# Kernel optimization log

Measured on AMD Instinct MI355X. Metric: run time of the kernel, lower is better.

Reference implementation:

```python
import jax, jax.numpy as jnp
import numpy as np

N, E, G, H = 4096, 8192, 64, 128  # nodes, edges, graphs, hidden dim
NODE_DIM, EDGE_DIM = 11, 5


def _linear_params(key, fan_in, fan_out):
    kw, kb = jax.random.split(key)
    s = 1.0 / np.sqrt(fan_in)
    w = jax.random.uniform(kw, (fan_in, fan_out), minval=-s, maxval=s, dtype=jnp.float32)
    b = jax.random.uniform(kb, (fan_out,), minval=-s, maxval=s, dtype=jnp.float32)
    return w, b


def setup_inputs() -> dict:
    key = jax.random.key(0)
    ks = jax.random.split(key, 10)
    x = jax.random.normal(ks[0], (N, NODE_DIM), dtype=jnp.float32)
    edge_attr = jax.random.normal(ks[1], (E, EDGE_DIM), dtype=jnp.float32)
    edge_index = jax.random.randint(ks[2], (2, E), 0, N, dtype=jnp.int64)
    batch = jnp.sort(jax.random.randint(ks[3], (N,), 0, G, dtype=jnp.int64))
    # preprocess MLP: node_dim -> 128 -> 128
    p1_w, p1_b = _linear_params(ks[4], NODE_DIM, H)
    p2_w, p2_b = _linear_params(ks[5], H, H)
    # edge net: edge_dim -> 128 -> 256 -> 128 -> 128*128 (ReLU between, none after last)
    e1_w, e1_b = _linear_params(ks[6], EDGE_DIM, 128)
    e2_w, e2_b = _linear_params(ks[7], 128, 256)
    e3_w, e3_b = _linear_params(ks[8], 256, 128)
    e4_w, e4_b = _linear_params(ks[9], 128, H * H)
    return {"x": x, "edge_attr": edge_attr, "edge_index": edge_index, "batch": batch,
            "p1_w": p1_w, "p1_b": p1_b, "p2_w": p2_w, "p2_b": p2_b,
            "e1_w": e1_w, "e1_b": e1_b, "e2_w": e2_w, "e2_b": e2_b,
            "e3_w": e3_w, "e3_b": e3_b, "e4_w": e4_w, "e4_b": e4_b}


def reference(x, edge_attr, edge_index, batch,
              p1_w, p1_b, p2_w, p2_b,
              e1_w, e1_b, e2_w, e2_b, e3_w, e3_b, e4_w, e4_b):
    # node preprocess MLP (maps 11-dim features to 128 so NNConv dims are consistent)
    h = jax.nn.relu(x @ p1_w + p1_b) @ p2_w + p2_b  # [N, H]
    # edge network -> per-edge weight matrix [E, H, H]
    e = jax.nn.relu(edge_attr @ e1_w + e1_b)
    e = jax.nn.relu(e @ e2_w + e2_b)
    e = jax.nn.relu(e @ e3_w + e3_b)
    W = (e @ e4_w + e4_b).reshape(E, H, H)
    # NNConv (root_weight=False, bias=False, aggr='mean'):
    src, dst = edge_index[0], edge_index[1]
    msg = jnp.einsum('ei,eio->eo', h[src], W)  # gather + per-edge matmul, [E, H]
    agg = jax.ops.segment_sum(msg, dst, num_segments=N)
    cnt = jax.ops.segment_sum(jnp.ones((E,), msg.dtype), dst, num_segments=N)
    h_out = agg / jnp.maximum(cnt, 1.0)[:, None]  # scatter-mean, [N, H]
    # global add pool over graphs
    pooled = jax.ops.segment_sum(h_out, batch, num_segments=G)  # [G, H]
    return pooled
```

## Files before the change

kernel.cpp:

```cpp
#include <hip/hip_runtime.h>
#include <stdint.h>
#include <stddef.h>

typedef unsigned short ushort_t;
typedef __attribute__((ext_vector_type(8))) short short8;
typedef __attribute__((ext_vector_type(4))) short short4v;
typedef __attribute__((ext_vector_type(4))) float f32x4;

#define GL2LDS(gsrc, ldst) \
  __builtin_amdgcn_global_load_lds((const __attribute__((address_space(1))) void*)(gsrc), \
                                   (__attribute__((address_space(3))) void*)(ldst), 16, 0, 0)

__device__ __forceinline__ float bf2f(ushort_t u) {
  union { unsigned int i; float f; } v; v.i = ((unsigned int)u) << 16; return v.f;
}
__device__ __forceinline__ ushort_t f2bf(float f) {
  unsigned int u = __builtin_bit_cast(unsigned int, f);
  unsigned int r = (u + 0x7fffu + ((u >> 16) & 1u)) >> 16;
  return (ushort_t)r;
}

__global__ void k_front(const float* __restrict__ e4w, const float* __restrict__ e4b,
                        ushort_t* __restrict__ e4wT,
                        const float* __restrict__ e2w, ushort_t* __restrict__ w2h,
                        ushort_t* __restrict__ w2l,
                        const float* __restrict__ e3w, ushort_t* __restrict__ w3h,
                        ushort_t* __restrict__ w3l,
                        const float* __restrict__ x, const float* __restrict__ p1w,
                        const float* __restrict__ p1b, const float* __restrict__ p2w,
                        const float* __restrict__ p2b, ushort_t* __restrict__ h_node) {
  __shared__ char smem[128 * 65 * 4];
  int bid = blockIdx.x, tid = threadIdx.x;

  if (bid < 258) {
    float (*t)[65] = (float(*)[65])smem;
    int c0 = bid * 64;
    for (int it = 0; it < 32; ++it) {
      int idx = it * 256 + tid;
      int cc = idx >> 7, oo = idx & 127;
      int c = c0 + cc;
      float v = (c < 16384) ? e4w[(size_t)c * 128 + oo] : e4b[(size_t)(c - 16384) * 128 + oo];
      t[oo][cc] = v;
    }
    __syncthreads();
    for (int it = 0; it < 32; ++it) {
      int idx = it * 256 + tid;
      int oo = idx >> 6, cc = idx & 63;
      e4wT[(size_t)oo * 16512 + c0 + cc] = f2bf(t[oo][cc]);
    }
  } else if (bid < 274) {
    int id = (bid - 258) * 256 + tid;
    int cf = id >> 8, ks = (id >> 6) & 3, ln = id & 63;
    int n = cf * 16 + (ln & 15);
    int k0 = (ks * 4 + (ln >> 4)) * 8;
    short8 ph, pl;
#pragma unroll
    for (int q = 0; q < 8; ++q) {
      float v = e2w[(size_t)(k0 + q) * 256 + n];
      ushort_t hb = f2bf(v);
      ph[q] = (short)hb;
      pl[q] = (short)f2bf(v - bf2f(hb));
    }
    *(short8*)(w2h + (size_t)id * 8) = ph;
    *(short8*)(w2l + (size_t)id * 8) = pl;
  } else if (bid < 290) {
    int id = (bid - 274) * 256 + tid;
    int cf = id >> 9, ks = (id >> 6) & 7, ln = id & 63;
    int n = cf * 16 + (ln & 15);
    int k0 = (ks * 4 + (ln >> 4)) * 8;
    short8 ph, pl;
#pragma unroll
    for (int q = 0; q < 8; ++q) {
      float v = e3w[(size_t)(k0 + q) * 128 + n];
      ushort_t hb = f2bf(v);
      ph[q] = (short)hb;
      pl[q] = (short)f2bf(v - bf2f(hb));
    }
    *(short8*)(w3h + (size_t)id * 8) = ph;
    *(short8*)(w3l + (size_t)id * 8) = pl;
  } else {
    float (*xs)[12] = (float(*)[12])smem;
    float (*t1)[128] = (float(*)[128])(smem + 8 * 12 * 4);
    int n0 = (bid - 290) * 8;
    if (tid < 88) { int n = tid / 11, j = tid % 11; xs[n][j] = x[(size_t)(n0 + n) * 11 + j]; }
    __syncthreads();
    for (int it = 0; it < 4; ++it) {
      int p = it * 256 + tid;
      int n = p >> 7, o = p & 127;
      float a = p1b[o];
#pragma unroll
      for (int j = 0; j < 11; ++j) a += xs[n][j] * p1w[j * 128 + o];
      t1[n][o] = fmaxf(a, 0.f);
    }
    __syncthreads();
    {
      int o = tid & 127, nb = tid >> 7;
      float a0 = p2b[o], a1_ = a0, a2_ = a0, a3_ = a0;
      for (int k4 = 0; k4 < 32; ++k4) {
        float w0 = p2w[(k4 * 4 + 0) * 128 + o];
        float w1 = p2w[(k4 * 4 + 1) * 128 + o];
        float w2 = p2w[(k4 * 4 + 2) * 128 + o];
        float w3 = p2w[(k4 * 4 + 3) * 128 + o];
        float4 v0 = *(const float4*)&t1[nb + 0][k4 * 4];
        float4 v1 = *(const float4*)&t1[nb + 2][k4 * 4];
        float4 v2 = *(const float4*)&t1[nb + 4][k4 * 4];
        float4 v3 = *(const float4*)&t1[nb + 6][k4 * 4];
        a0 += v0.x * w0 + v0.y * w1 + v0.z * w2 + v0.w * w3;
        a1_ += v1.x * w0 + v1.y * w1 + v1.z * w2 + v1.w * w3;
        a2_ += v2.x * w0 + v2.y * w1 + v2.z * w2 + v2.w * w3;
        a3_ += v3.x * w0 + v3.y * w1 + v3.z * w2 + v3.w * w3;
      }
      h_node[(size_t)(n0 + nb + 0) * 128 + o] = f2bf(a0);
      h_node[(size_t)(n0 + nb + 2) * 128 + o] = f2bf(a1_);
      h_node[(size_t)(n0 + nb + 4) * 128 + o] = f2bf(a2_);
      h_node[(size_t)(n0 + nb + 6) * 128 + o] = f2bf(a3_);
    }
  }
}

__global__ void k_mlp(const float* __restrict__ ea,
                      const float* __restrict__ e1w, const float* __restrict__ e1b,
                      const ushort_t* __restrict__ w2h, const ushort_t* __restrict__ w2l,
                      const float* __restrict__ e2b,
                      const ushort_t* __restrict__ w3h, const ushort_t* __restrict__ w3l,
                      const float* __restrict__ e3b,
                      float* __restrict__ e3Tf) {
  __shared__ float eas[32][6];
  __shared__ ushort_t a1h[32 * 136], a1l[32 * 136];
  __shared__ ushort_t a2h[32 * 264], a2l[32 * 264];
  __shared__ float a3t[128 * 40];

  int tid = threadIdx.x;
  int w = tid >> 6, ln = tid & 63, g = ln >> 4, l15 = ln & 15;
  int e0 = blockIdx.x * 32;

  if (tid < 160) { int n = tid / 5, j = tid % 5; eas[n][j] = ea[(size_t)(e0 + n) * 5 + j]; }
  __syncthreads();

  {
    int n = tid >> 4, ob = (tid & 15) * 8;
    float acc1[8];
    float4 ba = *(const float4*)(e1b + ob);
    float4 bb = *(const float4*)(e1b + ob + 4);
    acc1[0] = ba.x; acc1[1] = ba.y; acc1[2] = ba.z; acc1[3] = ba.w;
    acc1[4] = bb.x; acc1[5] = bb.y; acc1[6] = bb.z; acc1[7] = bb.w;
#pragma unroll
    for (int j = 0; j < 5; ++j) {
      float aj = eas[n][j];
      float4 wa = *(const float4*)(e1w + j * 128 + ob);
      float4 wb = *(const float4*)(e1w + j * 128 + ob + 4);
      acc1[0] = fmaf(aj, wa.x, acc1[0]); acc1[1] = fmaf(aj, wa.y, acc1[1]);
      acc1[2] = fmaf(aj, wa.z, acc1[2]); acc1[3] = fmaf(aj, wa.w, acc1[3]);
      acc1[4] = fmaf(aj, wb.x, acc1[4]); acc1[5] = fmaf(aj, wb.y, acc1[5]);
      acc1[6] = fmaf(aj, wb.z, acc1[6]); acc1[7] = fmaf(aj, wb.w, acc1[7]);
    }
    short8 ph, pl;
#pragma unroll
    for (int q = 0; q < 8; ++q) {
      float v = fmaxf(acc1[q], 0.f);
      ushort_t hb = f2bf(v);
      ph[q] = (short)hb;
      pl[q] = (short)f2bf(v - bf2f(hb));
    }
    int addr = n * 136 + ob;
    *(short8*)(a1h + addr) = ph;
    *(short8*)(a1l + addr) = pl;
  }
  __syncthreads();

  {
    f32x4 acc2[2][2];
#pragma unroll
    for (int rf = 0; rf < 2; ++rf)
#pragma unroll
      for (int cf = 0; cf < 2; ++cf) acc2[rf][cf] = (f32x4){0.f, 0.f, 0.f, 0.f};
    short8 ah[2][4], al[2][4];
#pragma unroll
    for (int rf = 0; rf < 2; ++rf)
#pragma unroll
      for (int ks = 0; ks < 4; ++ks) {
        int row = rf * 16 + l15;
        int addr = row * 136 + (ks * 4 + g) * 8;
        ah[rf][ks] = *(const short8*)(a1h + addr);
        al[rf][ks] = *(const short8*)(a1l + addr);
      }
#pragma unroll
    for (int ks = 0; ks < 4; ++ks) {
#pragma unroll
      for (int cfi = 0; cfi < 2; ++cfi) {
        int cf = w * 2 + cfi;
        size_t poff = (size_t)(((cf * 4 + ks) << 6) + ln) * 8;
        short8 bh = *(const short8*)(w2h + poff);
        short8 bl = *(const short8*)(w2l + poff);
#pragma unroll
        for (int rf = 0; rf < 2; ++rf) {
          acc2[rf][cfi] = __builtin_amdgcn_mfma_f32_16x16x32_bf16(ah[rf][ks], bh, acc2[rf][cfi], 0, 0, 0);
          acc2[rf][cfi] = __builtin_amdgcn_mfma_f32_16x16x32_bf16(al[rf][ks], bh, acc2[rf][cfi], 0, 0, 0);
          acc2[rf][cfi] = __builtin_amdgcn_mfma_f32_16x16x32_bf16(ah[rf][ks], bl, acc2[rf][cfi], 0, 0, 0);
        }
      }
    }
#pragma unroll
    for (int rf = 0; rf < 2; ++rf)
#pragma unroll
      for (int cfi = 0; cfi < 2; ++cfi) {
        int col = (w * 2 + cfi) * 16 + l15;
        float b = e2b[col];
#pragma unroll
        for (int r2 = 0; r2 < 4; ++r2) {
          int row = rf * 16 + g * 4 + r2;
          float v = fmaxf(acc2[rf][cfi][r2] + b, 0.f);
          ushort_t hb = f2bf(v);
          int addr = row * 264 + col;
          a2h[addr] = hb;
          a2l[addr] = f2bf(v - bf2f(hb));
        }
      }
  }
  __syncthreads();

  {
    f32x4 acc3[2];
    acc3[0] = (f32x4){0.f, 0.f, 0.f, 0.f};
    acc3[1] = (f32x4){0.f, 0.f, 0.f, 0.f};
#pragma unroll
    for (int ks = 0; ks < 8; ++ks) {
      short8 a2hf[2], a2lf[2];
#pragma unroll
      for (int rf = 0; rf < 2; ++rf) {
        int row = rf * 16 + l15;
        int addr = row * 264 + (ks * 4 + g) * 8;
        a2hf[rf] = *(const short8*)(a2h + addr);
        a2lf[rf] = *(const short8*)(a2l + addr);
      }
      size_t poff = (size_t)(((w * 8 + ks) << 6) + ln) * 8;
      short8 bh = *(const short8*)(w3h + poff);
      short8 bl = *(const short8*)(w3l + poff);
#pragma unroll
      for (int rf = 0; rf < 2; ++rf) {
        acc3[rf] = __builtin_amdgcn_mfma_f32_16x16x32_bf16(a2hf[rf], bh, acc3[rf], 0, 0, 0);
        acc3[rf] = __builtin_amdgcn_mfma_f32_16x16x32_bf16(a2lf[rf], bh, acc3[rf], 0, 0, 0);
        acc3[rf] = __builtin_amdgcn_mfma_f32_16x16x32_bf16(a2hf[rf], bl, acc3[rf], 0, 0, 0);
      }
    }
    int col = w * 16 + l15;
    float b = e3b[col];
#pragma unroll
    for (int rf = 0; rf < 2; ++rf)
#pragma unroll
      for (int r2 = 0; r2 < 4; ++r2) {
        int row = rf * 16 + g * 4 + r2;
        float v = fmaxf(acc3[rf][r2] + b, 0.f);
        a3t[col * 40 + row] = v;
      }
  }
  __syncthreads();

  {
    int o = tid >> 2, eq = (tid & 3) * 8;
    float4 q0 = *(const float4*)(a3t + o * 40 + eq);
    float4 q1 = *(const float4*)(a3t + o * 40 + eq + 4);
    *(float4*)(e3Tf + (size_t)o * 8192 + e0 + eq) = q0;
    *(float4*)(e3Tf + (size_t)o * 8192 + e0 + eq + 4) = q1;
  }
}

__launch_bounds__(512, 1)
__global__ void k_gemm(const ushort_t* __restrict__ h_node, const int* __restrict__ eidx,
                       const float* __restrict__ e3Tf,
                       const ushort_t* __restrict__ e4wT, ushort_t* __restrict__ partial) {
  __shared__ ushort_t bufA[16384];
  __shared__ float e3s[32 * 128];

  int tid = threadIdx.x;
  int w = tid >> 6, ln = tid & 63;
  int g = ln >> 4, l15 = ln & 15;
  int bid = blockIdx.x;
  int mt = bid >> 2, s = bid & 3;
  int e0 = mt * 128;
  int t0 = s * 32;
  int nt = (s == 3) ? 33 : 32;

  {
#pragma unroll
    for (int it = 0; it < 4; ++it) {
      int chunk = it * 512 + tid;
      int r = chunk >> 4;
      int Gt = (chunk & 15) ^ (r & 15);
      int se = eidx[e0 + r];
      GL2LDS(h_node + (size_t)se * 128 + Gt * 8, (char*)&bufA[0] + (it * 512 + w * 64) * 16);
    }
#pragma unroll
    for (int it = 0; it < 2; ++it) {
      int chunk = it * 512 + tid;
      int tl = chunk >> 5, cc = chunk & 31;
      GL2LDS(e3Tf + (size_t)(t0 + tl) * 8192 + e0 + cc * 4,
             (char*)&e3s[0] + (it * 512 + w * 64) * 16);
    }
  }
  asm volatile("s_waitcnt vmcnt(0)" ::: "memory");
  __builtin_amdgcn_s_barrier();
  asm volatile("" ::: "memory");

  short8 afr[8][4];
#pragma unroll
  for (int rf = 0; rf < 8; ++rf)
#pragma unroll
    for (int ks = 0; ks < 4; ++ks) {
      int row = rf * 16 + l15;
      int gr = (ks * 4 + g) ^ (row & 15);
      afr[rf][ks] = *(const short8*)((const char*)&bufA[0] + row * 256 + gr * 16);
    }

  f32x4 acc[8];
#pragma unroll
  for (int rf = 0; rf < 8; ++rf) acc[rf] = (f32x4){0.f, 0.f, 0.f, 0.f};

  const f32x4 zero4 = {0.f, 0.f, 0.f, 0.f};
  int nrow = w * 16 + l15;

  const ushort_t* brow = e4wT + (size_t)nrow * 16512 + (size_t)t0 * 128;
  short8 bcur[4], bnxt[4];
#pragma unroll
  for (int ks = 0; ks < 4; ++ks) bcur[ks] = *(const short8*)(brow + (ks * 4 + g) * 8);
  brow += 128;

  for (int tl = 0; tl < nt; ++tl) {
    int tg = t0 + tl;

    if (tl + 1 < nt) {
#pragma unroll
      for (int ks = 0; ks < 4; ++ks) bnxt[ks] = *(const short8*)(brow + (ks * 4 + g) * 8);
      brow += 128;
    }

    f32x4 part[8];
#pragma unroll
    for (int rf = 0; rf < 8; ++rf)
      part[rf] = __builtin_amdgcn_mfma_f32_16x16x32_bf16(afr[rf][0], bcur[0], zero4, 0, 0, 0);
#pragma unroll
    for (int ks = 1; ks < 4; ++ks)
#pragma unroll
      for (int rf = 0; rf < 8; ++rf)
        part[rf] = __builtin_amdgcn_mfma_f32_16x16x32_bf16(afr[rf][ks], bcur[ks], part[rf], 0, 0, 0);

    if (tg < 128) {
#pragma unroll
      for (int rf = 0; rf < 8; ++rf) {
        float4 ev = *(const float4*)&e3s[tl * 128 + rf * 16 + g * 4];
        acc[rf][0] = fmaf(ev.x, part[rf][0], acc[rf][0]);
        acc[rf][1] = fmaf(ev.y, part[rf][1], acc[rf][1]);
        acc[rf][2] = fmaf(ev.z, part[rf][2], acc[rf][2]);
        acc[rf][3] = fmaf(ev.w, part[rf][3], acc[rf][3]);
      }
    } else {
#pragma unroll
      for (int rf = 0; rf < 8; ++rf)
#pragma unroll
        for (int r2 = 0; r2 < 4; ++r2) acc[rf][r2] += part[rf][r2];
    }

    if (tl + 1 < nt) {
#pragma unroll
      for (int ks = 0; ks < 4; ++ks) bcur[ks] = bnxt[ks];
    }
  }

#pragma unroll
  for (int rf = 0; rf < 8; ++rf)
#pragma unroll
    for (int r2 = 0; r2 < 4; ++r2) {
      int row = rf * 16 + g * 4 + r2;
      partial[((size_t)s * 8192 + e0 + row) * 128 + nrow] = f2bf(acc[rf][r2]);
    }
}

__global__ void k_reduce(const ushort_t* __restrict__ partial, const int* __restrict__ eidx,
                         float* __restrict__ agg, float* __restrict__ cnt) {
  int id = blockIdx.x * 256 + threadIdx.x;
  int e = id >> 4, oc = (id & 15) * 8;
  float v[8];
#pragma unroll
  for (int q = 0; q < 8; ++q) v[q] = 0.f;
#pragma unroll
  for (int s2 = 0; s2 < 4; ++s2) {
    short8 p = *(const short8*)(partial + ((size_t)s2 * 8192 + e) * 128 + oc);
#pragma unroll
    for (int q = 0; q < 8; ++q) v[q] += bf2f((ushort_t)p[q]);
  }
  int d = eidx[8192 + e];
  float* dst = agg + (size_t)d * 128 + oc;
#pragma unroll
  for (int q = 0; q < 8; ++q) atomicAdd(dst + q, v[q]);
  if ((id & 15) == 0) atomicAdd(&cnt[d], 1.0f);
}

__device__ __forceinline__ int lbound(const int* a, int n, int v) {
  int lo = 0, hi = n;
  while (lo < hi) { int m = (lo + hi) >> 1; if (a[m] < v) lo = m + 1; else hi = m; }
  return lo;
}

__global__ void k_pool(const float* __restrict__ agg, const float* __restrict__ cnt,
                       const int* __restrict__ batch, float* __restrict__ out) {
  int gph = blockIdx.x, o = threadIdx.x;
  int lo = lbound(batch, 4096, gph);
  int hi = lbound(batch, 4096, gph + 1);
  float a = 0.f;
  for (int n = lo; n < hi; ++n) a += agg[(size_t)n * 128 + o] / fmaxf(cnt[n], 1.0f);
  out[(size_t)gph * 128 + o] = a;
}

extern "C" void kernel_launch(void* const* d_in, const int* in_sizes, int n_in,
                              void* d_out, int out_size, void* d_ws, size_t ws_size,
                              hipStream_t stream) {
  (void)in_sizes; (void)n_in; (void)out_size; (void)ws_size;
  const float* x   = (const float*)d_in[0];
  const float* ea  = (const float*)d_in[1];
  const int*   ei  = (const int*)d_in[2];
  const int*   bat = (const int*)d_in[3];
  const float* p1w = (const float*)d_in[4];  const float* p1b = (const float*)d_in[5];
  const float* p2w = (const float*)d_in[6];  const float* p2b = (const float*)d_in[7];
  const float* e1w = (const float*)d_in[8];  const float* e1b = (const float*)d_in[9];
  const float* e2w = (const float*)d_in[10]; const float* e2b = (const float*)d_in[11];
  const float* e3w = (const float*)d_in[12]; const float* e3b = (const float*)d_in[13];
  const float* e4w = (const float*)d_in[14]; const float* e4b = (const float*)d_in[15];

  char* ws = (char*)d_ws;
  ushort_t* e4wT   = (ushort_t*)(ws + 0);
  ushort_t* h_node = (ushort_t*)(ws + 4227072);
  float*    e3Tf   = (float*)(ws + 5275648);
  ushort_t* part   = (ushort_t*)(ws + 9469952);
  float*    agg    = (float*)(ws + 17858560);
  float*    cnt    = (float*)(ws + 19955712);
  ushort_t* w2h    = (ushort_t*)(ws + 19972096);
  ushort_t* w2l    = (ushort_t*)(ws + 20037632);
  ushort_t* w3h    = (ushort_t*)(ws + 20103168);
  ushort_t* w3l    = (ushort_t*)(ws + 20168704);

  hipMemsetAsync(ws + 17858560, 0, 2097152 + 16384, stream);

  k_front <<<802,  256, 0, stream>>>(e4w, e4b, e4wT, e2w, w2h, w2l, e3w, w3h, w3l,
                                     x, p1w, p1b, p2w, p2b, h_node);
  k_mlp   <<<256,  512, 0, stream>>>(ea, e1w, e1b, w2h, w2l, e2b,
                                     w3h, w3l, e3b, e3Tf);
  k_gemm  <<<256,  512, 0, stream>>>(h_node, ei, e3Tf, e4wT, part);
  k_reduce<<<512,  256, 0, stream>>>(part, ei, agg, cnt);
  k_pool  <<<64,   128, 0, stream>>>(agg, cnt, bat, (float*)d_out);
}
```

Measured before the change: 204.5 us.

## Retile edge GEMM to 64-edge blocks with 16 waves split 2x8

Halves the edge tile per block from 128 to 64 rows and raises the block to 1024 threads (16 waves arranged 2 along edges by 8 along output columns), doubling the grid to 512 blocks. Each wave now holds 2 A fragments instead of 8, cutting register pressure and raising occupancy across the CUs. The cost is that every B fragment of the large e4wT weight is now streamed by twice as many blocks, so there is less reuse of the weight per load and more global/L2 traffic.

```diff
diff --git a/kernel.cpp b/kernel.cpp
--- a/kernel.cpp
+++ b/kernel.cpp
@@ -265,89 +265,86 @@
   }
 }
 
-__launch_bounds__(512, 1)
+__launch_bounds__(1024, 4)
 __global__ void k_gemm(const ushort_t* __restrict__ h_node, const int* __restrict__ eidx,
                        const float* __restrict__ e3Tf,
                        const ushort_t* __restrict__ e4wT, ushort_t* __restrict__ partial) {
-  __shared__ ushort_t bufA[16384];
-  __shared__ float e3s[32 * 128];
+  __shared__ ushort_t bufA[8192];
+  __shared__ float e3s[32 * 64];
 
   int tid = threadIdx.x;
-  int w = tid >> 6, ln = tid & 63;
+  int wv = tid >> 6;
+  int wm = wv >> 3;
+  int wn = wv & 7;
+  int ln = tid & 63;
   int g = ln >> 4, l15 = ln & 15;
   int bid = blockIdx.x;
   int mt = bid >> 2, s = bid & 3;
-  int e0 = mt * 128;
+  int e0 = mt * 64;
   int t0 = s * 32;
   int nt = (s == 3) ? 33 : 32;
 
   {
-#pragma unroll
-    for (int it = 0; it < 4; ++it) {
-      int chunk = it * 512 + tid;
-      int r = chunk >> 4;
-      int Gt = (chunk & 15) ^ (r & 15);
-      int se = eidx[e0 + r];
-      GL2LDS(h_node + (size_t)se * 128 + Gt * 8, (char*)&bufA[0] + (it * 512 + w * 64) * 16);
-    }
-#pragma unroll
-    for (int it = 0; it < 2; ++it) {
-      int chunk = it * 512 + tid;
-      int tl = chunk >> 5, cc = chunk & 31;
+    int r = tid >> 4;
+    int Gt = (tid & 15) ^ (r & 15);
+    int se = eidx[e0 + r];
+    GL2LDS(h_node + (size_t)se * 128 + Gt * 8, (char*)&bufA[0] + (tid & ~63) * 16);
+    if (tid < 512) {
+      int tl = tid >> 4, cc = tid & 15;
       GL2LDS(e3Tf + (size_t)(t0 + tl) * 8192 + e0 + cc * 4,
-             (char*)&e3s[0] + (it * 512 + w * 64) * 16);
+             (char*)&e3s[0] + (tid & ~63) * 16);
     }
   }
   asm volatile("s_waitcnt vmcnt(0)" ::: "memory");
   __builtin_amdgcn_s_barrier();
   asm volatile("" ::: "memory");
 
-  short8 afr[8][4];
-#pragma unroll
-  for (int rf = 0; rf < 8; ++rf)
+  short8 afr[2][4];
+#pragma unroll
+  for (int rf = 0; rf < 2; ++rf)
 #pragma unroll
     for (int ks = 0; ks < 4; ++ks) {
-      int row = rf * 16 + l15;
+      int row = wm * 32 + rf * 16 + l15;
       int gr = (ks * 4 + g) ^ (row & 15);
       afr[rf][ks] = *(const short8*)((const char*)&bufA[0] + row * 256 + gr * 16);
     }
 
-  f32x4 acc[8];
-#pragma unroll
-  for (int rf = 0; rf < 8; ++rf) acc[rf] = (f32x4){0.f, 0.f, 0.f, 0.f};
+  f32x4 acc[2];
+  acc[0] = (f32x4){0.f, 0.f, 0.f, 0.f};
+  acc[1] = (f32x4){0.f, 0.f, 0.f, 0.f};
 
   const f32x4 zero4 = {0.f, 0.f, 0.f, 0.f};
-  int nrow = w * 16 + l15;
-
-  const ushort_t* brow = e4wT + (size_t)nrow * 16512 + (size_t)t0 * 128;
+  int nrow = wn * 16 + l15;
+
+  const ushort_t* bp = e4wT + (size_t)nrow * 16512 + (size_t)t0 * 128 + g * 8;
   short8 bcur[4], bnxt[4];
 #pragma unroll
-  for (int ks = 0; ks < 4; ++ks) bcur[ks] = *(const short8*)(brow + (ks * 4 + g) * 8);
-  brow += 128;
+  for (int ks = 0; ks < 4; ++ks) bcur[ks] = *(const short8*)(bp + ks * 32);
 
   for (int tl = 0; tl < nt; ++tl) {
     int tg = t0 + tl;
-
-    if (tl + 1 < nt) {
-#pragma unroll
-      for (int ks = 0; ks < 4; ++ks) bnxt[ks] = *(const short8*)(brow + (ks * 4 + g) * 8);
-      brow += 128;
-    }
-
-    f32x4 part[8];
-#pragma unroll
-    for (int rf = 0; rf < 8; ++rf)
+    bool more = (tl + 1 < nt);
+
+    if (more) {
+      const ushort_t* bq = bp + (size_t)(tl + 1) * 128;
+#pragma unroll
+      for (int ks = 0; ks < 4; ++ks) bnxt[ks] = *(const short8*)(bq + ks * 32);
+    }
+
+    f32x4 part[2];
+#pragma unroll
+    for (int rf = 0; rf < 2; ++rf)
       part[rf] = __builtin_amdgcn_mfma_f32_16x16x32_bf16(afr[rf][0], bcur[0], zero4, 0, 0, 0);
 #pragma unroll
     for (int ks = 1; ks < 4; ++ks)
 #pragma unroll
-      for (int rf = 0; rf < 8; ++rf)
+      for (int rf = 0; rf < 2; ++rf)
         part[rf] = __builtin_amdgcn_mfma_f32_16x16x32_bf16(afr[rf][ks], bcur[ks], part[rf], 0, 0, 0);
 
     if (tg < 128) {
 #pragma unroll
-      for (int rf = 0; rf < 8; ++rf) {
-        float4 ev = *(const float4*)&e3s[tl * 128 + rf * 16 + g * 4];
+      for (int rf = 0; rf < 2; ++rf) {
+        float4 ev = *(const float4*)&e3s[tl * 64 + wm * 32 + rf * 16 + g * 4];
         acc[rf][0] = fmaf(ev.x, part[rf][0], acc[rf][0]);
         acc[rf][1] = fmaf(ev.y, part[rf][1], acc[rf][1]);
         acc[rf][2] = fmaf(ev.z, part[rf][2], acc[rf][2]);
@@ -355,22 +352,22 @@
       }
     } else {
 #pragma unroll
-      for (int rf = 0; rf < 8; ++rf)
+      for (int rf = 0; rf < 2; ++rf)
 #pragma unroll
         for (int r2 = 0; r2 < 4; ++r2) acc[rf][r2] += part[rf][r2];
     }
 
-    if (tl + 1 < nt) {
+    if (more) {
 #pragma unroll
       for (int ks = 0; ks < 4; ++ks) bcur[ks] = bnxt[ks];
     }
   }
 
 #pragma unroll
-  for (int rf = 0; rf < 8; ++rf)
+  for (int rf = 0; rf < 2; ++rf)
 #pragma unroll
     for (int r2 = 0; r2 < 4; ++r2) {
-      int row = rf * 16 + g * 4 + r2;
+      int row = wm * 32 + rf * 16 + g * 4 + r2;
       partial[((size_t)s * 8192 + e0 + row) * 128 + nrow] = f2bf(acc[rf][r2]);
     }
 }
@@ -440,11 +437,11 @@
 
   hipMemsetAsync(ws + 17858560, 0, 2097152 + 16384, stream);
 
-  k_front <<<802,  256, 0, stream>>>(e4w, e4b, e4wT, e2w, w2h, w2l, e3w, w3h, w3l,
-                                     x, p1w, p1b, p2w, p2b, h_node);
-  k_mlp   <<<256,  512, 0, stream>>>(ea, e1w, e1b, w2h, w2l, e2b,
-                                     w3h, w3l, e3b, e3Tf);
-  k_gemm  <<<256,  512, 0, stream>>>(h_node, ei, e3Tf, e4wT, part);
-  k_reduce<<<512,  256, 0, stream>>>(part, ei, agg, cnt);
-  k_pool  <<<64,   128, 0, stream>>>(agg, cnt, bat, (float*)d_out);
-}
+  k_front <<<802,  256,  0, stream>>>(e4w, e4b, e4wT, e2w, w2h, w2l, e3w, w3h, w3l,
+                                      x, p1w, p1b, p2w, p2b, h_node);
+  k_mlp   <<<256,  512,  0, stream>>>(ea, e1w, e1b, w2h, w2l, e2b,
+                                      w3h, w3l, e3b, e3Tf);
+  k_gemm  <<<512,  1024, 0, stream>>>(h_node, ei, e3Tf, e4wT, part);
+  k_reduce<<<512,  256,  0, stream>>>(part, ei, agg, cnt);
+  k_pool  <<<64,   128,  0, stream>>>(agg, cnt, bat, (float*)d_out);
+}
```

New measurement: 288.3 us. 41.0% more time.

## Fuse scatter-add into GEMM epilogue and move edge counting into front kernel

Applied to the files above, without the earlier changes.

The GEMM kernel now atomically adds its fp32 per-edge partial results directly into the node aggregation buffer, using destination indices cached in shared memory. This removes the bf16 partial buffer round trip and the separate reduce kernel launch. Edge-count atomics move into extra blocks of the front kernel. The cost is four times more float atomics to global memory, one from each column split, but partials are no longer rounded to bf16 before summation.

```diff
diff --git a/kernel.cpp b/kernel.cpp
--- a/kernel.cpp
+++ b/kernel.cpp
@@ -28,7 +28,8 @@
                         ushort_t* __restrict__ w3l,
                         const float* __restrict__ x, const float* __restrict__ p1w,
                         const float* __restrict__ p1b, const float* __restrict__ p2w,
-                        const float* __restrict__ p2b, ushort_t* __restrict__ h_node) {
+                        const float* __restrict__ p2b, ushort_t* __restrict__ h_node,
+                        const int* __restrict__ eidx, float* __restrict__ cnt) {
   __shared__ char smem[128 * 65 * 4];
   int bid = blockIdx.x, tid = threadIdx.x;
 
@@ -78,7 +79,7 @@
     }
     *(short8*)(w3h + (size_t)id * 8) = ph;
     *(short8*)(w3l + (size_t)id * 8) = pl;
-  } else {
+  } else if (bid < 802) {
     float (*xs)[12] = (float(*)[12])smem;
     float (*t1)[128] = (float(*)[128])(smem + 8 * 12 * 4);
     int n0 = (bid - 290) * 8;
@@ -115,6 +116,9 @@
       h_node[(size_t)(n0 + nb + 4) * 128 + o] = f2bf(a2_);
       h_node[(size_t)(n0 + nb + 6) * 128 + o] = f2bf(a3_);
     }
+  } else {
+    int e = (bid - 802) * 256 + tid;
+    atomicAdd(&cnt[eidx[8192 + e]], 1.0f);
   }
 }
 
@@ -268,9 +272,10 @@
 __launch_bounds__(512, 1)
 __global__ void k_gemm(const ushort_t* __restrict__ h_node, const int* __restrict__ eidx,
                        const float* __restrict__ e3Tf,
-                       const ushort_t* __restrict__ e4wT, ushort_t* __restrict__ partial) {
+                       const ushort_t* __restrict__ e4wT, float* __restrict__ agg) {
   __shared__ ushort_t bufA[16384];
   __shared__ float e3s[32 * 128];
+  __shared__ int dsts[128];
 
   int tid = threadIdx.x;
   int w = tid >> 6, ln = tid & 63;
@@ -281,6 +286,7 @@
   int t0 = s * 32;
   int nt = (s == 3) ? 33 : 32;
 
+  if (tid < 128) dsts[tid] = eidx[8192 + e0 + tid];
   {
 #pragma unroll
     for (int it = 0; it < 4; ++it) {
@@ -371,28 +377,9 @@
 #pragma unroll
     for (int r2 = 0; r2 < 4; ++r2) {
       int row = rf * 16 + g * 4 + r2;
-      partial[((size_t)s * 8192 + e0 + row) * 128 + nrow] = f2bf(acc[rf][r2]);
-    }
-}
-
-__global__ void k_reduce(const ushort_t* __restrict__ partial, const int* __restrict__ eidx,
-                         float* __restrict__ agg, float* __restrict__ cnt) {
-  int id = blockIdx.x * 256 + threadIdx.x;
-  int e = id >> 4, oc = (id & 15) * 8;
-  float v[8];
-#pragma unroll
-  for (int q = 0; q < 8; ++q) v[q] = 0.f;
-#pragma unroll
-  for (int s2 = 0; s2 < 4; ++s2) {
-    short8 p = *(const short8*)(partial + ((size_t)s2 * 8192 + e) * 128 + oc);
-#pragma unroll
-    for (int q = 0; q < 8; ++q) v[q] += bf2f((ushort_t)p[q]);
-  }
-  int d = eidx[8192 + e];
-  float* dst = agg + (size_t)d * 128 + oc;
-#pragma unroll
-  for (int q = 0; q < 8; ++q) atomicAdd(dst + q, v[q]);
-  if ((id & 15) == 0) atomicAdd(&cnt[d], 1.0f);
+      int d = dsts[row];
+      atomicAdd(&agg[(size_t)d * 128 + nrow], acc[rf][r2]);
+    }
 }
 
 __device__ __forceinline__ int lbound(const int* a, int n, int v) {
@@ -430,21 +417,19 @@
   ushort_t* e4wT   = (ushort_t*)(ws + 0);
   ushort_t* h_node = (ushort_t*)(ws + 4227072);
   float*    e3Tf   = (float*)(ws + 5275648);
-  ushort_t* part   = (ushort_t*)(ws + 9469952);
-  float*    agg    = (float*)(ws + 17858560);
-  float*    cnt    = (float*)(ws + 19955712);
-  ushort_t* w2h    = (ushort_t*)(ws + 19972096);
-  ushort_t* w2l    = (ushort_t*)(ws + 20037632);
-  ushort_t* w3h    = (ushort_t*)(ws + 20103168);
-  ushort_t* w3l    = (ushort_t*)(ws + 20168704);
-
-  hipMemsetAsync(ws + 17858560, 0, 2097152 + 16384, stream);
-
-  k_front <<<802,  256, 0, stream>>>(e4w, e4b, e4wT, e2w, w2h, w2l, e3w, w3h, w3l,
-                                     x, p1w, p1b, p2w, p2b, h_node);
+  float*    agg    = (float*)(ws + 9469952);
+  float*    cnt    = (float*)(ws + 11567104);
+  ushort_t* w2h    = (ushort_t*)(ws + 11583488);
+  ushort_t* w2l    = (ushort_t*)(ws + 11649024);
+  ushort_t* w3h    = (ushort_t*)(ws + 11714560);
+  ushort_t* w3l    = (ushort_t*)(ws + 11780096);
+
+  hipMemsetAsync(ws + 9469952, 0, 2097152 + 16384, stream);
+
+  k_front <<<834,  256, 0, stream>>>(e4w, e4b, e4wT, e2w, w2h, w2l, e3w, w3h, w3l,
+                                     x, p1w, p1b, p2w, p2b, h_node, ei, cnt);
   k_mlp   <<<256,  512, 0, stream>>>(ea, e1w, e1b, w2h, w2l, e2b,
                                      w3h, w3l, e3b, e3Tf);
-  k_gemm  <<<256,  512, 0, stream>>>(h_node, ei, e3Tf, e4wT, part);
-  k_reduce<<<512,  256, 0, stream>>>(part, ei, agg, cnt);
+  k_gemm  <<<256,  512, 0, stream>>>(h_node, ei, e3Tf, e4wT, agg);
   k_pool  <<<64,   128, 0, stream>>>(agg, cnt, bat, (float*)d_out);
 }
```

Measured after the change: 180.0 us. 1.14x faster.
